# Optimization experiments

Hardware: AMD Instinct MI355X
Metric: run time of the kernel (lower is better)

Reference implementation:

```python
import jax, jax.numpy as jnp
import numpy as np

B, S, IN, H, D, M, OUT, TOPK = 4, 256, 256, 512, 128, 100000, 256, 3
EPS = 1e-12  # F.normalize eps


def _l2norm(x):
    n = jnp.sqrt(jnp.sum(x * x, axis=-1, keepdims=True))
    return x / jnp.maximum(n, EPS)


def setup_inputs() -> dict:
    key = jax.random.key(0)
    ks = jax.random.split(key, 16)
    s = 0.02
    return {
        "x": jax.random.normal(ks[0], (B, S, IN), jnp.float32),
        # LSTM params (torch gate order i,f,g,o)
        "W_ih": jax.random.normal(ks[1], (4 * H, IN), jnp.float32) * s,
        "W_hh": jax.random.normal(ks[2], (4 * H, H), jnp.float32) * s,
        "b_ih": jax.random.normal(ks[3], (4 * H,), jnp.float32) * s,
        "b_hh": jax.random.normal(ks[4], (4 * H,), jnp.float32) * s,
        # memory interface
        "Wq": jax.random.normal(ks[5], (D, H), jnp.float32) * s,
        "bq": jax.random.normal(ks[6], (D,), jnp.float32) * s,
        "Wa": jax.random.normal(ks[7], (1, D), jnp.float32) * s,
        "ba": jax.random.normal(ks[8], (1,), jnp.float32) * s,
        "Wc": jax.random.normal(ks[9], (D, D), jnp.float32) * s,
        "bc": jax.random.normal(ks[10], (D,), jnp.float32) * s,
        # output layer
        "Wo": jax.random.normal(ks[11], (OUT, H + D), jnp.float32) * s,
        "bo": jax.random.normal(ks[12], (OUT,), jnp.float32) * s,
        # memory bank (importance_weight == 1.0 for all fresh entries)
        "mem_keys": jax.random.normal(ks[13], (M, D), jnp.float32),
        "mem_values": jax.random.normal(ks[14], (M, D), jnp.float32),
    }


def _lstm(x, W_ih, W_hh, b_ih, b_hh):
    b = b_ih + b_hh
    xg = jnp.einsum('bsi,gi->bsg', x, W_ih) + b  # (B,S,4H)

    def step(carry, xg_t):
        h, c = carry
        g = xg_t + h @ W_hh.T
        i, f, gg, o = jnp.split(g, 4, axis=-1)
        c = jax.nn.sigmoid(f) * c + jax.nn.sigmoid(i) * jnp.tanh(gg)
        h = jax.nn.sigmoid(o) * jnp.tanh(c)
        return (h, c), h

    h0 = jnp.zeros((x.shape[0], W_hh.shape[1]), x.dtype)
    (_, _), hs = jax.lax.scan(step, (h0, h0), jnp.swapaxes(xg, 0, 1))
    return jnp.swapaxes(hs, 0, 1)  # (B,S,H)


def reference(x, W_ih, W_hh, b_ih, b_hh, Wq, bq, Wa, ba, Wc, bc, Wo, bo, mem_keys, mem_values):
    h = _lstm(x, W_ih, W_hh, b_ih, b_hh)               # (B,S,H)
    q = _l2norm(h @ Wq.T + bq)                          # (B,S,D) normalized query
    kn = _l2norm(mem_keys)                              # (M,D)
    sims = jnp.einsum('bsd,md->bsm', q, kn)             # cosine sims (x1.0 importance)
    _, idx = jax.lax.top_k(sims, TOPK)                  # (B,S,K)
    retrieved = mem_values[idx]                         # (B,S,K,D) gather
    att = jax.nn.softmax(jnp.squeeze(retrieved @ Wa.T + ba, -1), axis=-1)  # (B,S,K)
    mem = jnp.einsum('bsk,bskd->bsd', att, retrieved)
    mem = mem @ Wc.T + bc                               # combine_layer
    out = jnp.concatenate([h, mem], axis=-1) @ Wo.T + bo  # (B,S,OUT)
    return out
```

## Files before the change

### kernel.cpp

```cpp
#include <hip/hip_runtime.h>
#include <math.h>

#define INF __builtin_inff()
#define SENT 0x7FA00000u
#define IMAX 0x7fffffff

typedef __attribute__((ext_vector_type(8))) short bhalf8;
typedef __attribute__((ext_vector_type(4))) float f32x4;


__device__ __forceinline__ void ins3b(float& v0, int& i0, float& v1, int& i1,
                                      float& v2, int& i2, float nv, int ni) {
  bool b0 = (nv > v0) || (nv == v0 && ni < i0);
  bool b1 = (nv > v1) || (nv == v1 && ni < i1);
  bool b2 = (nv > v2) || (nv == v2 && ni < i2);
  v2 = b1 ? v1 : (b2 ? nv : v2);
  i2 = b1 ? i1 : (b2 ? ni : i2);
  v1 = b0 ? v0 : (b1 ? nv : v1);
  i1 = b0 ? i0 : (b1 ? ni : i1);
  v0 = b0 ? nv : v0;
  i0 = b0 ? ni : i0;
}

__device__ __forceinline__ unsigned short f2bf(float x) {
  unsigned u = __float_as_uint(x);
  return (unsigned short)((u + 0x7FFFu + ((u >> 16) & 1u)) >> 16);
}

__global__ void init_k(float* __restrict__ h_seq) {
  int t = blockIdx.x * 256 + threadIdx.x;
  if (t < 526336) h_seq[t] = (t < 2048) ? 0.f : __uint_as_float(SENT);
}

template<int AMODE>
__global__ __launch_bounds__(256) void gemm_k(
    const float* __restrict__ A, const float* __restrict__ A2,
    const float* __restrict__ Bw, const float* __restrict__ b1,
    const float* __restrict__ b2, float* __restrict__ C,
    int M, int N, int K) {
  __shared__ float4 As4[64][16];
  __shared__ float4 Bs4[64][16];
  const int t = threadIdx.x;
  const int tx = t & 15, ty = t >> 4;
  const int brow = blockIdx.x * 64, bcol = blockIdx.y * 64;
  const int srow = t >> 2, scb = t & 3;
  float acc[4][4] = {};
  for (int kt = 0; kt < K; kt += 64) {
#pragma unroll
    for (int u = 0; u < 4; ++u) {
      int c = scb + 4 * u;
      int gk = kt + c * 4;
      int gr = brow + srow;
      const float* ap;
      if (AMODE == 0) {
        ap = A + (size_t)gr * K + gk;
      } else {
        int b = gr >> 8, s = gr & 255;
        const float* hrow = A + ((size_t)(s + 1) * 4 + b) * 512;
        if (AMODE == 1) ap = hrow + gk;
        else ap = (gk < 512) ? (hrow + gk) : (A2 + (size_t)gr * 128 + (gk - 512));
      }
      As4[srow][c ^ (srow & 15)] = *(const float4*)ap;
      Bs4[srow][c ^ (srow & 15)] = *(const float4*)(Bw + (size_t)(bcol + srow) * K + gk);
    }
    __syncthreads();
#pragma unroll
    for (int d4 = 0; d4 < 16; ++d4) {
      float4 av[4], bv[4];
#pragma unroll
      for (int i = 0; i < 4; ++i) av[i] = As4[ty * 4 + i][d4 ^ ((ty * 4 + i) & 15)];
#pragma unroll
      for (int j = 0; j < 4; ++j) bv[j] = Bs4[tx * 4 + j][d4 ^ ((tx * 4 + j) & 15)];
#pragma unroll
      for (int i = 0; i < 4; ++i)
#pragma unroll
        for (int j = 0; j < 4; ++j)
          acc[i][j] += av[i].x * bv[j].x + av[i].y * bv[j].y +
                       av[i].z * bv[j].z + av[i].w * bv[j].w;
    }
    __syncthreads();
  }
#pragma unroll
  for (int i = 0; i < 4; ++i) {
    int r = brow + ty * 4 + i;
#pragma unroll
    for (int j = 0; j < 4; ++j) {
      int n = bcol + tx * 4 + j;
      float bias = b1[n];
      if (b2) bias += b2[n];
      C[(size_t)r * N + n] = acc[i][j] + bias;
    }
  }
}

__global__ __launch_bounds__(1024, 4) void lstm_k(
    const float* __restrict__ xg, const float* __restrict__ W_hh,
    float* __restrict__ h_seq) {
  const int bid = blockIdx.x;
  const int batch = bid >> 4;
  const int ub = bid & 15;
  const int t = threadIdx.x;
  const int gp = t >> 9;
  const int tin = t & 511;
  const int uu = tin >> 4;
  const int li = tin & 15;
  const int unit = ub * 32 + uu;
  __shared__ float h_lds[16 * 36];
  __shared__ float go_lds[32][2];

  float w[2][32];
#pragma unroll
  for (int g2 = 0; g2 < 2; ++g2) {
    const float* wr = W_hh + (size_t)((gp * 2 + g2) * 512 + unit) * 512 + li * 32;
#pragma unroll
    for (int j = 0; j < 32; j += 4) {
      float4 v = *(const float4*)(wr + j);
      w[g2][j] = v.x; w[g2][j + 1] = v.y; w[g2][j + 2] = v.z; w[g2][j + 3] = v.w;
    }
  }
  float c = 0.f;
  float xgv[2];
#pragma unroll
  for (int g2 = 0; g2 < 2; ++g2)
    xgv[g2] = xg[(size_t)(batch * 256) * 2048 + (gp * 2 + g2) * 512 + unit];

  for (int step = 0; step < 256; ++step) {
    if (t < 512) {
      const float* hp = h_seq + ((size_t)step * 4 + batch) * 512 + t;
      float hv;
      do {
        hv = __hip_atomic_load(hp, __ATOMIC_RELAXED, __HIP_MEMORY_SCOPE_AGENT);
      } while (__float_as_uint(hv) == SENT);
      h_lds[((t >> 5) * 36) + (t & 31)] = hv;
    }
    __syncthreads();
    float a0 = 0.f, a1 = 0.f;
#pragma unroll
    for (int j = 0; j < 32; j += 4) {
      float4 hv = *(const float4*)(&h_lds[li * 36 + j]);
      a0 += w[0][j] * hv.x + w[0][j + 1] * hv.y + w[0][j + 2] * hv.z + w[0][j + 3] * hv.w;
      a1 += w[1][j] * hv.x + w[1][j + 1] * hv.y + w[1][j + 2] * hv.z + w[1][j + 3] * hv.w;
    }
#pragma unroll
    for (int m = 1; m < 16; m <<= 1) {
      a0 += __shfl_xor(a0, m, 64);
      a1 += __shfl_xor(a1, m, 64);
    }
    a0 += xgv[0]; a1 += xgv[1];
    if (gp == 1 && li == 0) { go_lds[uu][0] = a0; go_lds[uu][1] = a1; }
    __syncthreads();
    if (step < 255) {
#pragma unroll
      for (int g2 = 0; g2 < 2; ++g2)
        xgv[g2] = xg[(size_t)(batch * 256 + step + 1) * 2048 + (gp * 2 + g2) * 512 + unit];
    }
    if (gp == 0) {
      float i_ = 1.f / (1.f + expf(-a0));
      float f_ = 1.f / (1.f + expf(-a1));
      float g_ = tanhf(go_lds[uu][0]);
      float o_ = 1.f / (1.f + expf(-go_lds[uu][1]));
      c = f_ * c + i_ * g_;
      float h = o_ * tanhf(c);
      if (li == 0)
        __hip_atomic_store(h_seq + ((size_t)(step + 1) * 4 + batch) * 512 + unit,
                           h, __ATOMIC_RELAXED, __HIP_MEMORY_SCOPE_AGENT);
    }
  }
}

__global__ __launch_bounds__(256) void qnorm_k(float* __restrict__ q,
                                               unsigned* __restrict__ qbf) {
  int wv = threadIdx.x >> 6, lane = threadIdx.x & 63;
  int r = blockIdx.x * 4 + wv;
  float2 v = *(float2*)(q + (size_t)r * 128 + lane * 2);
  float ss = v.x * v.x + v.y * v.y;
#pragma unroll
  for (int m = 1; m < 64; m <<= 1) ss += __shfl_xor(ss, m, 64);
  float inv = 1.f / fmaxf(sqrtf(ss), 1e-12f);
  v.x *= inv; v.y *= inv;
  *(float2*)(q + (size_t)r * 128 + lane * 2) = v;
  qbf[(size_t)r * 64 + lane] = (unsigned)f2bf(v.x) | ((unsigned)f2bf(v.y) << 16);
}

__global__ __launch_bounds__(256) void convk_k(const float* __restrict__ keys,
                                               float* __restrict__ invn,
                                               unsigned* __restrict__ kbf) {
  int wv = threadIdx.x >> 6, lane = threadIdx.x & 63;
  int r = blockIdx.x * 4 + wv;
  float2 v = *(const float2*)(keys + (size_t)r * 128 + lane * 2);
  float ss = v.x * v.x + v.y * v.y;
#pragma unroll
  for (int m = 1; m < 64; m <<= 1) ss += __shfl_xor(ss, m, 64);
  float inv = 1.f / fmaxf(sqrtf(ss), 1e-12f);
  if (lane == 0) invn[r] = inv;
  kbf[(size_t)r * 64 + lane] =
      (unsigned)f2bf(v.x * inv) | ((unsigned)f2bf(v.y * inv) << 16);
}

__device__ __forceinline__ void stage_tile(unsigned short* dst,
                                           const unsigned* src,
                                           int baserow, int maxrow,
                                           int w, int l) {
#pragma unroll
  for (int u = 0; u < 4; ++u) {
    int s = u * 256 + w * 64 + l;
    int row = s >> 4, cc = s & 15;
    int gr = baserow + row; gr = gr > maxrow ? maxrow : gr;
    const unsigned* sp = src + (size_t)gr * 64 + ((cc ^ (row & 7)) << 2);
    __builtin_amdgcn_global_load_lds(
        (const __attribute__((address_space(1))) unsigned*)sp,
        (__attribute__((address_space(3))) unsigned*)(dst + (size_t)(u * 256 + w * 64) * 8),
        16, 0, 0);
  }
}

__global__ __launch_bounds__(256, 2) void simsmfma_k(
    const unsigned* __restrict__ qbf, const unsigned* __restrict__ kbf,
    float* __restrict__ pvals, int* __restrict__ pidx) {
  const int qt = blockIdx.x, ch = blockIdx.y;
  const int kbeg = ch * 3125, klim = kbeg + 3125;
  const int t = threadIdx.x, l = t & 63, w = t >> 6;
  __shared__ alignas(16) unsigned short ks0[8192];
  __shared__ alignas(16) unsigned short ks1[8192];

  stage_tile(ks1, qbf, qt * 64, 1023, w, l);
  __syncthreads();
  bhalf8 afrag[4];
  {
    int row = w * 16 + (l & 15);
#pragma unroll
    for (int db = 0; db < 4; ++db) {
      int cslot = db * 4 + (l >> 4);
      afrag[db] = *(const bhalf8*)&ks1[(size_t)(row * 16 + (cslot ^ (row & 7))) * 8];
    }
  }
  stage_tile(ks0, kbf, kbeg, klim - 1, w, l);
  __syncthreads();

  float tv0[4], tv1[4], tv2[4]; int ti0[4], ti1[4], ti2[4];
#pragma unroll
  for (int r = 0; r < 4; ++r) {
    tv0[r] = tv1[r] = tv2[r] = -INF;
    ti0[r] = ti1[r] = ti2[r] = IMAX;
  }

  for (int s = 0; s < 49; ++s) {
    unsigned short* cur = (s & 1) ? ks1 : ks0;
    unsigned short* nxt = (s & 1) ? ks0 : ks1;
    if (s < 48) stage_tile(nxt, kbf, kbeg + (s + 1) * 64, klim - 1, w, l);
    int k0 = kbeg + s * 64;

    f32x4 ac0 = {0,0,0,0}, ac1 = {0,0,0,0}, ac2 = {0,0,0,0}, ac3 = {0,0,0,0};
    const int r0 = l & 15;
#pragma unroll
    for (int db = 0; db < 4; ++db) {
      int swz = (db * 4 + (l >> 4)) ^ (r0 & 7);
      bhalf8 b0 = *(const bhalf8*)&cur[(size_t)((r0     ) * 16 + swz) * 8];
      bhalf8 b1 = *(const bhalf8*)&cur[(size_t)((r0 + 16) * 16 + swz) * 8];
      bhalf8 b2 = *(const bhalf8*)&cur[(size_t)((r0 + 32) * 16 + swz) * 8];
      bhalf8 b3 = *(const bhalf8*)&cur[(size_t)((r0 + 48) * 16 + swz) * 8];
      ac0 = __builtin_amdgcn_mfma_f32_16x16x32_bf16(afrag[db], b0, ac0, 0, 0, 0);
      ac1 = __builtin_amdgcn_mfma_f32_16x16x32_bf16(afrag[db], b1, ac1, 0, 0, 0);
      ac2 = __builtin_amdgcn_mfma_f32_16x16x32_bf16(afrag[db], b2, ac2, 0, 0, 0);
      ac3 = __builtin_amdgcn_mfma_f32_16x16x32_bf16(afrag[db], b3, ac3, 0, 0, 0);
    }
#pragma unroll
    for (int nt = 0; nt < 4; ++nt) {
      f32x4 a = (nt == 0) ? ac0 : (nt == 1) ? ac1 : (nt == 2) ? ac2 : ac3;
      int gk = k0 + nt * 16 + (l & 15);
      bool ok = gk < klim;
#pragma unroll
      for (int r = 0; r < 4; ++r) {
        float v = ok ? a[r] : -INF;
        ins3b(tv0[r], ti0[r], tv1[r], ti1[r], tv2[r], ti2[r], v, gk);
      }
    }
    __syncthreads();
  }

#pragma unroll
  for (int r = 0; r < 4; ++r) {
    float c0 = tv0[r], c1 = tv1[r], c2 = tv2[r];
    int j0 = ti0[r], j1 = ti1[r], j2 = ti2[r];
    int qrow = qt * 64 + w * 16 + (l >> 4) * 4 + r;
    size_t ob = ((size_t)ch * 1024 + qrow) * 6;
#pragma unroll
    for (int e = 0; e < 6; ++e) {
      float mv = c0; int mi = j0;
#pragma unroll
      for (int m = 1; m < 16; m <<= 1) {
        float o = __shfl_xor(mv, m, 64); int oi = __shfl_xor(mi, m, 64);
        bool tk = (o > mv) || (o == mv && oi < mi);
        mv = tk ? o : mv; mi = tk ? oi : mi;
      }
      if (mi == j0) { c0 = c1; j0 = j1; c1 = c2; j1 = j2; c2 = -INF; j2 = IMAX; }
      if ((l & 15) == 0) { pvals[ob + e] = mv; pidx[ob + e] = mi; }
    }
  }
}

__global__ __launch_bounds__(256) void merge_rescore_k(
    const float* __restrict__ pvals, const int* __restrict__ pidx,
    const float* __restrict__ qf, const float* __restrict__ keys,
    const float* __restrict__ invn, const float* __restrict__ mvals,
    const float* __restrict__ Wa, const float* __restrict__ ba,
    float* __restrict__ mem_pre) {
  int wv = threadIdx.x >> 6, l = threadIdx.x & 63;
  int qr = blockIdx.x * 4 + wv;
  float h0 = -INF, h1 = -INF, h2 = -INF;
  int g0 = IMAX, g1 = IMAX, g2 = IMAX;
#pragma unroll
  for (int e = 0; e < 3; ++e) {
    int c = l * 3 + e;
    size_t base = ((size_t)(c / 6) * 1024 + qr) * 6 + (c % 6);
    ins3b(h0, g0, h1, g1, h2, g2, pvals[base], pidx[base]);
  }
  float sc[8]; int si[8];
#pragma unroll
  for (int e = 0; e < 8; ++e) {
    float mv = h0; int mi = g0;
#pragma unroll
    for (int m = 1; m < 64; m <<= 1) {
      float o = __shfl_xor(mv, m, 64); int oi = __shfl_xor(mi, m, 64);
      bool tk = (o > mv) || (o == mv && oi < mi);
      mv = tk ? o : mv; mi = tk ? oi : mi;
    }
    sc[e] = mv; si[e] = mi;
    if (mi == g0) { h0 = h1; g0 = g1; h1 = h2; g1 = g2; h2 = -INF; g2 = IMAX; }
  }
  int d = l * 2;
  float q0 = qf[(size_t)qr * 128 + d], q1 = qf[(size_t)qr * 128 + d + 1];
  float ex[8];
#pragma unroll
  for (int e = 0; e < 8; ++e) {
    int k = si[e];
    float p = q0 * keys[(size_t)k * 128 + d] + q1 * keys[(size_t)k * 128 + d + 1];
#pragma unroll
    for (int m = 1; m < 64; m <<= 1) p += __shfl_xor(p, m, 64);
    ex[e] = p * invn[k];
  }
  float v0 = -INF, v1 = -INF, v2 = -INF;
  int i0 = IMAX, i1 = IMAX, i2 = IMAX;
#pragma unroll
  for (int e = 0; e < 8; ++e) ins3b(v0, i0, v1, i1, v2, i2, ex[e], si[e]);
  float r00 = mvals[(size_t)i0 * 128 + d], r01 = mvals[(size_t)i0 * 128 + d + 1];
  float r10 = mvals[(size_t)i1 * 128 + d], r11 = mvals[(size_t)i1 * 128 + d + 1];
  float r20 = mvals[(size_t)i2 * 128 + d], r21 = mvals[(size_t)i2 * 128 + d + 1];
  float wa0 = Wa[d], wa1 = Wa[d + 1];
  float p0 = wa0 * r00 + wa1 * r01;
  float p1 = wa0 * r10 + wa1 * r11;
  float p2 = wa0 * r20 + wa1 * r21;
#pragma unroll
  for (int m = 1; m < 64; m <<= 1) {
    p0 += __shfl_xor(p0, m, 64);
    p1 += __shfl_xor(p1, m, 64);
    p2 += __shfl_xor(p2, m, 64);
  }
  float bav = ba[0];
  float l0 = p0 + bav, l1 = p1 + bav, l2 = p2 + bav;
  float mx = fmaxf(l0, fmaxf(l1, l2));
  float e0 = expf(l0 - mx), e1 = expf(l1 - mx), e2 = expf(l2 - mx);
  float s = e0 + e1 + e2;
  float a0 = e0 / s, a1 = e1 / s, a2 = e2 / s;
  mem_pre[(size_t)qr * 128 + d]     = a0 * r00 + a1 * r10 + a2 * r20;
  mem_pre[(size_t)qr * 128 + d + 1] = a0 * r01 + a1 * r11 + a2 * r21;
}

extern "C" void kernel_launch(void* const* d_in, const int* in_sizes, int n_in,
                              void* d_out, int out_size, void* d_ws, size_t ws_size,
                              hipStream_t stream) {
  (void)in_sizes; (void)n_in; (void)out_size; (void)ws_size;
  const float* x    = (const float*)d_in[0];
  const float* W_ih = (const float*)d_in[1];
  const float* W_hh = (const float*)d_in[2];
  const float* b_ih = (const float*)d_in[3];
  const float* b_hh = (const float*)d_in[4];
  const float* Wq   = (const float*)d_in[5];
  const float* bq   = (const float*)d_in[6];
  const float* Wa   = (const float*)d_in[7];
  const float* ba   = (const float*)d_in[8];
  const float* Wc   = (const float*)d_in[9];
  const float* bc   = (const float*)d_in[10];
  const float* Wo   = (const float*)d_in[11];
  const float* bo   = (const float*)d_in[12];
  const float* keys = (const float*)d_in[13];
  const float* vals = (const float*)d_in[14];

  float* ws      = (float*)d_ws;
  float* xg      = ws + 0;
  float* h_seq   = ws + 2097152;
  float* qbuf    = ws + 2623488;
  float* invn    = ws + 2754560;
  float* mem_pre = ws + 2854560;
  float* mem_cmb = ws + 2985632;
  float* pvals   = ws + 3116704;
  int*   pidx    = (int*)(ws + 3313312);
  unsigned* qbf  = (unsigned*)(ws + 3509920);
  unsigned* kbf  = (unsigned*)(ws + 3575456);

  init_k<<<2056, 256, 0, stream>>>(h_seq);
  gemm_k<0><<<dim3(16, 32), 256, 0, stream>>>(x, nullptr, W_ih, b_ih, b_hh, xg,
                                              1024, 2048, 256);
  convk_k<<<25000, 256, 0, stream>>>(keys, invn, kbf);
  lstm_k<<<64, 1024, 0, stream>>>(xg, W_hh, h_seq);
  gemm_k<1><<<dim3(16, 2), 256, 0, stream>>>(h_seq, nullptr, Wq, bq, nullptr,
                                             qbuf, 1024, 128, 512);
  qnorm_k<<<256, 256, 0, stream>>>(qbuf, qbf);
  simsmfma_k<<<dim3(16, 32), 256, 0, stream>>>(qbf, kbf, pvals, pidx);
  merge_rescore_k<<<256, 256, 0, stream>>>(pvals, pidx, qbuf, keys, invn, vals,
                                           Wa, ba, mem_pre);
  gemm_k<0><<<dim3(16, 2), 256, 0, stream>>>(mem_pre, nullptr, Wc, bc, nullptr,
                                             mem_cmb, 1024, 128, 128);
  gemm_k<2><<<dim3(16, 4), 256, 0, stream>>>(h_seq, mem_cmb, Wo, bo, nullptr,
                                             (float*)d_out, 1024, 256, 640);
}
```

Measured before the change: 1.210 ms.

## Fuse input GEMM, LSTM recurrence and key normalization into one persistent kernel

Merges the xg input-projection GEMM, the LSTM recurrence and the memory-key normalization into a single launch with role-split blocks. LSTM blocks spin on sentinel-initialized xg entries, so the recurrence can start while the GEMM blocks are still producing later timesteps, and key conversion runs alongside. The LSTM block shrinks to 512 threads, with each thread computing all four gates in registers, and h is double-buffered in LDS, which drops the cross-group LDS exchange. The cost is a larger sentinel init pass over the whole xg buffer. Correctness also depends on the spinning LSTM blocks being co-resident with the producer blocks, otherwise the kernel can deadlock.

Measured after the change: 1.159 ms. 4.2% less time.

```diff
diff --git a/kernel.cpp b/kernel.cpp
--- a/kernel.cpp
+++ b/kernel.cpp
@@ -27,9 +27,12 @@
   return (unsigned short)((u + 0x7FFFu + ((u >> 16) & 1u)) >> 16);
 }
 
-__global__ void init_k(float* __restrict__ h_seq) {
+__global__ void init_k(float* __restrict__ base) {
   int t = blockIdx.x * 256 + threadIdx.x;
-  if (t < 526336) h_seq[t] = (t < 2048) ? 0.f : __uint_as_float(SENT);
+  if (t < 2623488) {
+    bool zero = (t >= 2097152) && (t < 2097152 + 2048);
+    base[t] = zero ? 0.f : __uint_as_float(SENT);
+  }
 }
 
 template<int AMODE>
@@ -93,77 +96,173 @@
   }
 }
 
-__global__ __launch_bounds__(1024, 4) void lstm_k(
-    const float* __restrict__ xg, const float* __restrict__ W_hh,
-    float* __restrict__ h_seq) {
+__global__ __launch_bounds__(512, 2) void fused_front(
+    const float* __restrict__ x, const float* __restrict__ W_ih,
+    const float* __restrict__ b_ih, const float* __restrict__ b_hh,
+    const float* __restrict__ W_hh, const float* __restrict__ keys,
+    float* __restrict__ xg, float* __restrict__ h_seq,
+    float* __restrict__ invn, unsigned* __restrict__ kbf) {
+  __shared__ alignas(16) unsigned char smem[32768];
   const int bid = blockIdx.x;
-  const int batch = bid >> 4;
-  const int ub = bid & 15;
   const int t = threadIdx.x;
-  const int gp = t >> 9;
-  const int tin = t & 511;
-  const int uu = tin >> 4;
-  const int li = tin & 15;
-  const int unit = ub * 32 + uu;
-  __shared__ float h_lds[16 * 36];
-  __shared__ float go_lds[32][2];
-
-  float w[2][32];
-#pragma unroll
-  for (int g2 = 0; g2 < 2; ++g2) {
-    const float* wr = W_hh + (size_t)((gp * 2 + g2) * 512 + unit) * 512 + li * 32;
-#pragma unroll
-    for (int j = 0; j < 32; j += 4) {
-      float4 v = *(const float4*)(wr + j);
-      w[g2][j] = v.x; w[g2][j + 1] = v.y; w[g2][j + 2] = v.z; w[g2][j + 3] = v.w;
-    }
-  }
-  float c = 0.f;
-  float xgv[2];
-#pragma unroll
-  for (int g2 = 0; g2 < 2; ++g2)
-    xgv[g2] = xg[(size_t)(batch * 256) * 2048 + (gp * 2 + g2) * 512 + unit];
-
-  for (int step = 0; step < 256; ++step) {
-    if (t < 512) {
-      const float* hp = h_seq + ((size_t)step * 4 + batch) * 512 + t;
-      float hv;
+
+  if (bid < 64) {
+    const int batch = bid >> 4;
+    const int ub = bid & 15;
+    const int uu = t >> 4;
+    const int li = t & 15;
+    const int unit = ub * 32 + uu;
+    float* h_lds = (float*)smem;
+
+    float w[4][32];
+#pragma unroll
+    for (int g = 0; g < 4; ++g) {
+      const float* wr = W_hh + (size_t)(g * 512 + unit) * 512 + li * 32;
+#pragma unroll
+      for (int j = 0; j < 32; j += 4) {
+        float4 v = *(const float4*)(wr + j);
+        w[g][j] = v.x; w[g][j + 1] = v.y; w[g][j + 2] = v.z; w[g][j + 3] = v.w;
+      }
+    }
+    float c = 0.f;
+    float xgv[4];
+    {
+      float* xq = xg + (size_t)(batch * 256) * 2048 + unit;
+      bool again;
       do {
-        hv = __hip_atomic_load(hp, __ATOMIC_RELAXED, __HIP_MEMORY_SCOPE_AGENT);
-      } while (__float_as_uint(hv) == SENT);
-      h_lds[((t >> 5) * 36) + (t & 31)] = hv;
-    }
-    __syncthreads();
-    float a0 = 0.f, a1 = 0.f;
-#pragma unroll
-    for (int j = 0; j < 32; j += 4) {
-      float4 hv = *(const float4*)(&h_lds[li * 36 + j]);
-      a0 += w[0][j] * hv.x + w[0][j + 1] * hv.y + w[0][j + 2] * hv.z + w[0][j + 3] * hv.w;
-      a1 += w[1][j] * hv.x + w[1][j + 1] * hv.y + w[1][j + 2] * hv.z + w[1][j + 3] * hv.w;
-    }
-#pragma unroll
-    for (int m = 1; m < 16; m <<= 1) {
-      a0 += __shfl_xor(a0, m, 64);
-      a1 += __shfl_xor(a1, m, 64);
-    }
-    a0 += xgv[0]; a1 += xgv[1];
-    if (gp == 1 && li == 0) { go_lds[uu][0] = a0; go_lds[uu][1] = a1; }
-    __syncthreads();
-    if (step < 255) {
-#pragma unroll
-      for (int g2 = 0; g2 < 2; ++g2)
-        xgv[g2] = xg[(size_t)(batch * 256 + step + 1) * 2048 + (gp * 2 + g2) * 512 + unit];
-    }
-    if (gp == 0) {
+        again = false;
+#pragma unroll
+        for (int g = 0; g < 4; ++g)
+          xgv[g] = __hip_atomic_load(xq + g * 512, __ATOMIC_RELAXED,
+                                     __HIP_MEMORY_SCOPE_AGENT);
+#pragma unroll
+        for (int g = 0; g < 4; ++g)
+          again |= (__float_as_uint(xgv[g]) == SENT);
+      } while (again);
+    }
+
+    for (int step = 0; step < 256; ++step) {
+      {
+        float* hp = h_seq + ((size_t)step * 4 + batch) * 512 + t;
+        float hv;
+        do {
+          hv = __hip_atomic_load(hp, __ATOMIC_RELAXED, __HIP_MEMORY_SCOPE_AGENT);
+        } while (__float_as_uint(hv) == SENT);
+        h_lds[(step & 1) * 576 + (t >> 5) * 36 + (t & 31)] = hv;
+      }
+      __syncthreads();
+      const float* hb = h_lds + (step & 1) * 576 + li * 36;
+      float a0 = 0.f, a1 = 0.f, a2 = 0.f, a3 = 0.f;
+#pragma unroll
+      for (int j = 0; j < 32; j += 4) {
+        float4 hv = *(const float4*)(hb + j);
+        a0 += w[0][j] * hv.x + w[0][j + 1] * hv.y + w[0][j + 2] * hv.z + w[0][j + 3] * hv.w;
+        a1 += w[1][j] * hv.x + w[1][j + 1] * hv.y + w[1][j + 2] * hv.z + w[1][j + 3] * hv.w;
+        a2 += w[2][j] * hv.x + w[2][j + 1] * hv.y + w[2][j + 2] * hv.z + w[2][j + 3] * hv.w;
+        a3 += w[3][j] * hv.x + w[3][j + 1] * hv.y + w[3][j + 2] * hv.z + w[3][j + 3] * hv.w;
+      }
+#pragma unroll
+      for (int m = 1; m < 16; m <<= 1) {
+        a0 += __shfl_xor(a0, m, 64); a1 += __shfl_xor(a1, m, 64);
+        a2 += __shfl_xor(a2, m, 64); a3 += __shfl_xor(a3, m, 64);
+      }
+      a0 += xgv[0]; a1 += xgv[1]; a2 += xgv[2]; a3 += xgv[3];
       float i_ = 1.f / (1.f + expf(-a0));
       float f_ = 1.f / (1.f + expf(-a1));
-      float g_ = tanhf(go_lds[uu][0]);
-      float o_ = 1.f / (1.f + expf(-go_lds[uu][1]));
+      float g_ = tanhf(a2);
+      float o_ = 1.f / (1.f + expf(-a3));
       c = f_ * c + i_ * g_;
       float h = o_ * tanhf(c);
       if (li == 0)
         __hip_atomic_store(h_seq + ((size_t)(step + 1) * 4 + batch) * 512 + unit,
                            h, __ATOMIC_RELAXED, __HIP_MEMORY_SCOPE_AGENT);
+      if (step < 255) {
+        float* xq = xg + (size_t)(batch * 256 + step + 1) * 2048 + unit;
+        bool again;
+        do {
+          again = false;
+#pragma unroll
+          for (int g = 0; g < 4; ++g)
+            xgv[g] = __hip_atomic_load(xq + g * 512, __ATOMIC_RELAXED,
+                                       __HIP_MEMORY_SCOPE_AGENT);
+#pragma unroll
+          for (int g = 0; g < 4; ++g)
+            again |= (__float_as_uint(xgv[g]) == SENT);
+        } while (again);
+      }
+    }
+  } else if (bid < 576) {
+    const int g = bid - 64;
+    const int q = g >> 7;
+    const int b = (g >> 5) & 3;
+    const int col = g & 31;
+    const int brow = (b * 4 + q) * 64, bcol = col * 64;
+    float4* As4 = (float4*)smem;
+    float4* Bs4 = (float4*)(smem + 16384);
+    const int tx = t & 15, ty = (t >> 4) & 15;
+    const int srow = (t & 255) >> 2, scb = t & 3;
+    float acc[4][4] = {};
+    for (int kt = 0; kt < 256; kt += 64) {
+      if (t < 256) {
+#pragma unroll
+        for (int u = 0; u < 4; ++u) {
+          int cc = scb + 4 * u;
+          int gk = kt + cc * 4;
+          As4[srow * 16 + (cc ^ (srow & 15))] =
+              *(const float4*)(x + (size_t)(brow + srow) * 256 + gk);
+          Bs4[srow * 16 + (cc ^ (srow & 15))] =
+              *(const float4*)(W_ih + (size_t)(bcol + srow) * 256 + gk);
+        }
+      }
+      __syncthreads();
+      if (t < 256) {
+#pragma unroll
+        for (int d4 = 0; d4 < 16; ++d4) {
+          float4 av[4], bv[4];
+#pragma unroll
+          for (int i = 0; i < 4; ++i)
+            av[i] = As4[(ty * 4 + i) * 16 + (d4 ^ ((ty * 4 + i) & 15))];
+#pragma unroll
+          for (int j = 0; j < 4; ++j)
+            bv[j] = Bs4[(tx * 4 + j) * 16 + (d4 ^ ((tx * 4 + j) & 15))];
+#pragma unroll
+          for (int i = 0; i < 4; ++i)
+#pragma unroll
+            for (int j = 0; j < 4; ++j)
+              acc[i][j] += av[i].x * bv[j].x + av[i].y * bv[j].y +
+                           av[i].z * bv[j].z + av[i].w * bv[j].w;
+        }
+      }
+      __syncthreads();
+    }
+    if (t < 256) {
+#pragma unroll
+      for (int i = 0; i < 4; ++i) {
+        int r = brow + ty * 4 + i;
+#pragma unroll
+        for (int j = 0; j < 4; ++j) {
+          int n = bcol + tx * 4 + j;
+          __hip_atomic_store(xg + (size_t)r * 2048 + n,
+                             acc[i][j] + b_ih[n] + b_hh[n],
+                             __ATOMIC_RELAXED, __HIP_MEMORY_SCOPE_AGENT);
+        }
+      }
+    }
+  } else {
+    const int rb = (bid - 576) * 256;
+    const int wv = t >> 6, lane = t & 63;
+    for (int p = 0; p < 32; ++p) {
+      int r = rb + p * 8 + wv;
+      if (r < 100000) {
+        float2 v = *(const float2*)(keys + (size_t)r * 128 + lane * 2);
+        float ss = v.x * v.x + v.y * v.y;
+#pragma unroll
+        for (int m = 1; m < 64; m <<= 1) ss += __shfl_xor(ss, m, 64);
+        float inv = 1.f / fmaxf(sqrtf(ss), 1e-12f);
+        if (lane == 0) invn[r] = inv;
+        kbf[(size_t)r * 64 + lane] =
+            (unsigned)f2bf(v.x * inv) | ((unsigned)f2bf(v.y * inv) << 16);
+      }
     }
   }
 }
@@ -180,21 +279,6 @@
   v.x *= inv; v.y *= inv;
   *(float2*)(q + (size_t)r * 128 + lane * 2) = v;
   qbf[(size_t)r * 64 + lane] = (unsigned)f2bf(v.x) | ((unsigned)f2bf(v.y) << 16);
-}
-
-__global__ __launch_bounds__(256) void convk_k(const float* __restrict__ keys,
-                                               float* __restrict__ invn,
-                                               unsigned* __restrict__ kbf) {
-  int wv = threadIdx.x >> 6, lane = threadIdx.x & 63;
-  int r = blockIdx.x * 4 + wv;
-  float2 v = *(const float2*)(keys + (size_t)r * 128 + lane * 2);
-  float ss = v.x * v.x + v.y * v.y;
-#pragma unroll
-  for (int m = 1; m < 64; m <<= 1) ss += __shfl_xor(ss, m, 64);
-  float inv = 1.f / fmaxf(sqrtf(ss), 1e-12f);
-  if (lane == 0) invn[r] = inv;
-  kbf[(size_t)r * 64 + lane] =
-      (unsigned)f2bf(v.x * inv) | ((unsigned)f2bf(v.y * inv) << 16);
 }
 
 __device__ __forceinline__ void stage_tile(unsigned short* dst,
@@ -398,11 +482,9 @@
   unsigned* qbf  = (unsigned*)(ws + 3509920);
   unsigned* kbf  = (unsigned*)(ws + 3575456);
 
-  init_k<<<2056, 256, 0, stream>>>(h_seq);
-  gemm_k<0><<<dim3(16, 32), 256, 0, stream>>>(x, nullptr, W_ih, b_ih, b_hh, xg,
-                                              1024, 2048, 256);
-  convk_k<<<25000, 256, 0, stream>>>(keys, invn, kbf);
-  lstm_k<<<64, 1024, 0, stream>>>(xg, W_hh, h_seq);
+  init_k<<<10248, 256, 0, stream>>>(ws);
+  fused_front<<<967, 512, 0, stream>>>(x, W_ih, b_ih, b_hh, W_hh, keys,
+                                       xg, h_seq, invn, kbf);
   gemm_k<1><<<dim3(16, 2), 256, 0, stream>>>(h_seq, nullptr, Wq, bq, nullptr,
                                              qbuf, 1024, 128, 512);
   qnorm_k<<<256, 256, 0, stream>>>(qbuf, qbf);
```
